# Performance work log

Measured on AMD Instinct MI355X. Metric: run time of the kernel, lower is better.

The kernel has to match this reference:

```python
import jax, jax.numpy as jnp
import numpy as np

T, N, F_IN, F_OUT, E = 12, 512, 32, 8, 16384
H = N * F_OUT  # 4096, LSTM input_size == hidden_size


def setup_inputs() -> dict:
    key = jax.random.key(0)
    ks = jax.random.split(key, 7)
    return {
        "x": jax.random.normal(ks[0], (T, N, F_IN), jnp.float32),
        "edge_index": jax.random.randint(ks[1], (T, 2, E), 0, N, jnp.int32),
        "edge_weight": jax.random.uniform(ks[2], (T, E), jnp.float32),
        "W_gcn": jax.random.normal(ks[3], (F_IN, F_OUT), jnp.float32) * 0.1,
        "b_gcn": jnp.zeros((F_OUT,), jnp.float32),
        "W_ih": jax.random.normal(ks[4], (4 * H, H), jnp.float32) * 0.02,
        "W_hh": jax.random.normal(ks[5], (4 * H, H), jnp.float32) * 0.02,
        "b_ih": jnp.zeros((4 * H,), jnp.float32),
        "b_hh": jnp.zeros((4 * H,), jnp.float32),
    }


def _gcn(x, ei, ew, W, b):
    # PyG GCNConv with edge_weight: add self loops (w=1), symmetric norm, scatter-add at target.
    row, col = ei[0], ei[1]
    loop = jnp.arange(N, dtype=ei.dtype)
    row = jnp.concatenate([row, loop])
    col = jnp.concatenate([col, loop])
    w = jnp.concatenate([ew, jnp.ones((N,), ew.dtype)])
    deg = jax.ops.segment_sum(w, col, num_segments=N)
    dinv = jnp.where(deg > 0, 1.0 / jnp.sqrt(jnp.where(deg > 0, deg, 1.0)), 0.0)
    norm = dinv[row] * w * dinv[col]  # [E+N]
    h = x @ W  # [N, F_OUT]
    out = jax.ops.segment_sum(norm[:, None] * h[row], col, num_segments=N)
    return out + b


def reference(x, edge_index, edge_weight, W_gcn, b_gcn, W_ih, W_hh, b_ih, b_hh):
    # Per-snapshot GCNConv -> relu (dropout is identity in eval mode)
    conv = jax.vmap(_gcn, in_axes=(0, 0, 0, None, None))(x, edge_index, edge_weight, W_gcn, b_gcn)
    feats = jax.nn.relu(conv).reshape(T, N * F_OUT)  # [T, H] LSTM inputs (batch=1)

    def step(carry, xt):
        h, c = carry
        g = xt @ W_ih.T + b_ih + h @ W_hh.T + b_hh  # [4H], torch gate order i,f,g,o
        i, f, gg, o = jnp.split(g, 4)
        c = jax.nn.sigmoid(f) * c + jax.nn.sigmoid(i) * jnp.tanh(gg)
        h = jax.nn.sigmoid(o) * jnp.tanh(c)
        return (h, c), None

    h0 = jnp.zeros((H,), x.dtype)
    c0 = jnp.zeros((H,), x.dtype)
    (h, c), _ = jax.lax.scan(step, (h0, c0), feats)
    # module returns (cell_state, hidden_state), each [1, H]
    return (c[None, :], h[None, :])
```

## Files before the change

### kernel.cpp

```cpp
#include <hip/hip_runtime.h>
#include <hip/hip_fp16.h>
#include <math.h>

#define T_STEPS 12
#define N_NODES 512
#define FIN 32
#define FOUT 8
#define E_EDGES 16384
#define HDIM 4096
#define H4 16384

__device__ __forceinline__ float sigmoidf_(float x) { return 1.0f / (1.0f + __expf(-x)); }

typedef float floatx4 __attribute__((ext_vector_type(4)));
__device__ __forceinline__ float4 ntload4(const float4* p) {
    floatx4 v = __builtin_nontemporal_load((const floatx4*)p);
    return make_float4(v.x, v.y, v.z, v.w);
}

__global__ __launch_bounds__(256) void gcn_kernel(
        const float* __restrict__ x,
        const int*   __restrict__ ei,
        const float* __restrict__ ew,
        const float* __restrict__ Wg,
        const float* __restrict__ bg,
        float* __restrict__ feats)
{
    const int t   = blockIdx.x;
    const int tid = threadIdx.x;

    __shared__ float hs[N_NODES * FOUT];
    __shared__ float outs[N_NODES * FOUT];
    __shared__ float deg[N_NODES];
    __shared__ float Wsh[FIN * FOUT];
    __shared__ float bsh[FOUT];

    const float* xt   = x  + (size_t)t * N_NODES * FIN;
    const int*   rowp = ei + (size_t)t * 2 * E_EDGES;
    const int*   colp = rowp + E_EDGES;
    const float* wp   = ew + (size_t)t * E_EDGES;

    if (tid < FIN * FOUT) Wsh[tid] = Wg[tid];
    if (tid < FOUT)       bsh[tid] = bg[tid];
    for (int i = tid; i < N_NODES; i += 256) deg[i] = 1.0f;
    for (int i = tid; i < N_NODES * FOUT; i += 256) outs[i] = 0.0f;
    __syncthreads();

    for (int idx = tid; idx < N_NODES * FOUT; idx += 256) {
        const int n = idx >> 3;
        const int f = idx & 7;
        const float* xr = xt + n * FIN;
        float acc = 0.0f;
        #pragma unroll
        for (int k = 0; k < FIN; ++k) acc += xr[k] * Wsh[k * FOUT + f];
        hs[idx] = acc;
    }
    for (int e = tid; e < E_EDGES; e += 256) atomicAdd(&deg[colp[e]], wp[e]);
    __syncthreads();

    for (int i = tid; i < N_NODES; i += 256) deg[i] = 1.0f / sqrtf(deg[i]);
    __syncthreads();

    for (int e = tid; e < E_EDGES; e += 256) {
        const int   r  = rowp[e];
        const int   cc = colp[e];
        const float coef = deg[r] * wp[e] * deg[cc];
        #pragma unroll
        for (int f = 0; f < FOUT; ++f)
            atomicAdd(&outs[cc * FOUT + f], coef * hs[r * FOUT + f]);
    }
    for (int n = tid; n < N_NODES; n += 256) {
        const float d2 = deg[n] * deg[n];
        #pragma unroll
        for (int f = 0; f < FOUT; ++f)
            atomicAdd(&outs[n * FOUT + f], d2 * hs[n * FOUT + f]);
    }
    __syncthreads();

    for (int idx = tid; idx < N_NODES * FOUT; idx += 256) {
        float v = outs[idx] + bsh[idx & 7];
        feats[(size_t)t * HDIM + idx] = v > 0.0f ? v : 0.0f;
    }
}

__global__ __launch_bounds__(256) void wih_gemm(
        const float* __restrict__ feats,
        const float* __restrict__ Wih,
        const float* __restrict__ b_ih,
        const float* __restrict__ b_hh,
        float* __restrict__ Xg)
{
    const int wave = threadIdx.x >> 6;
    const int lane = threadIdx.x & 63;
    const int r0   = blockIdx.x * 8 + wave * 2;

    const float4* W4 = (const float4*)Wih;
    const float4* F4 = (const float4*)feats;

    float acc0[T_STEPS], acc1[T_STEPS];
    #pragma unroll
    for (int t = 0; t < T_STEPS; ++t) { acc0[t] = 0.0f; acc1[t] = 0.0f; }

    #pragma unroll 1
    for (int ch = 0; ch < 16; ++ch) {
        const int k4 = ch * 64 + lane;
        const float4 w0 = ntload4(&W4[(size_t)r0 * (HDIM / 4) + k4]);
        const float4 w1 = ntload4(&W4[(size_t)(r0 + 1) * (HDIM / 4) + k4]);
        #pragma unroll
        for (int t = 0; t < T_STEPS; ++t) {
            const float4 fv = F4[t * (HDIM / 4) + k4];
            acc0[t] += w0.x * fv.x + w0.y * fv.y + w0.z * fv.z + w0.w * fv.w;
            acc1[t] += w1.x * fv.x + w1.y * fv.y + w1.z * fv.z + w1.w * fv.w;
        }
    }

    const float bias0 = b_ih[r0] + b_hh[r0];
    const float bias1 = b_ih[r0 + 1] + b_hh[r0 + 1];

    #pragma unroll
    for (int t = 0; t < T_STEPS; ++t) {
        float v0 = acc0[t], v1 = acc1[t];
        #pragma unroll
        for (int off = 32; off > 0; off >>= 1) {
            v0 += __shfl_xor(v0, off, 64);
            v1 += __shfl_xor(v1, off, 64);
        }
        if (lane == 0) {
            Xg[t * H4 + r0]     = v0 + bias0;
            Xg[t * H4 + r0 + 1] = v1 + bias1;
        }
    }
}

__global__ __launch_bounds__(256) void lstm_step0(
        const float* __restrict__ Xg0,
        float* __restrict__ h_out,
        float* __restrict__ c)
{
    const int j = blockIdx.x * 256 + threadIdx.x;
    const float gi = Xg0[j];
    const float gg = Xg0[2 * HDIM + j];
    const float go = Xg0[3 * HDIM + j];
    const float cj = sigmoidf_(gi) * tanhf(gg);
    c[j] = cj;
    h_out[j] = sigmoidf_(go) * tanhf(cj);
}

__global__ __launch_bounds__(256) void lstm_step_cvt(
        const float* __restrict__ Xg_t,
        const float* __restrict__ Whh,
        uint4* __restrict__ Whh16,
        const float* __restrict__ h_in,
        float* __restrict__ h_out,
        float* __restrict__ c)
{
    const int j    = blockIdx.x;
    const int wave = threadIdx.x >> 6;
    const int lane = threadIdx.x & 63;
    const int r    = wave * HDIM + j;

    const float xg    = (lane == 0) ? Xg_t[r] : 0.0f;
    const float cprev = (threadIdx.x == 0) ? c[j] : 0.0f;

    const float4* Wr  = (const float4*)(Whh + (size_t)r * HDIM);
    uint4*        Wo  = Whh16 + (size_t)r * (HDIM / 8);
    const float4* h4  = (const float4*)h_in;

    float acc = 0.0f;
    #pragma unroll
    for (int it = 0; it < 8; ++it) {
        const int g = it * 64 + lane;
        const float4 a  = ntload4(&Wr[2 * g]);
        const float4 b  = ntload4(&Wr[2 * g + 1]);
        const float4 ha = h4[2 * g];
        const float4 hb = h4[2 * g + 1];
        acc += a.x * ha.x + a.y * ha.y + a.z * ha.z + a.w * ha.w
             + b.x * hb.x + b.y * hb.y + b.z * hb.z + b.w * hb.w;
        union { uint4 u; __half2 h[4]; } pk;
        pk.h[0] = __floats2half2_rn(a.x, a.y);
        pk.h[1] = __floats2half2_rn(a.z, a.w);
        pk.h[2] = __floats2half2_rn(b.x, b.y);
        pk.h[3] = __floats2half2_rn(b.z, b.w);
        Wo[g] = pk.u;
    }
    #pragma unroll
    for (int off = 32; off > 0; off >>= 1) acc += __shfl_xor(acc, off, 64);

    __shared__ float gate[4];
    if (lane == 0) gate[wave] = acc + xg;
    __syncthreads();

    if (threadIdx.x == 0) {
        const float gi = gate[0], gf = gate[1], gg = gate[2], go = gate[3];
        const float cj = sigmoidf_(gf) * cprev + sigmoidf_(gi) * tanhf(gg);
        const float hj = sigmoidf_(go) * tanhf(cj);
        c[j] = cj;
        h_out[j] = hj;
    }
}

__global__ __launch_bounds__(256) void lstm_step_f16(
        const float* __restrict__ Xg_t,
        const uint4* __restrict__ Whh16,
        const float* __restrict__ h_in,
        float* __restrict__ h_out,
        float* __restrict__ c,
        float* __restrict__ final_out)
{
    const int j    = blockIdx.x;
    const int wave = threadIdx.x >> 6;
    const int lane = threadIdx.x & 63;
    const int r    = wave * HDIM + j;

    const float xg    = (lane == 0) ? Xg_t[r] : 0.0f;
    const float cprev = (threadIdx.x == 0) ? c[j] : 0.0f;

    const uint4*  Wr = Whh16 + (size_t)r * (HDIM / 8);
    const float4* h4 = (const float4*)h_in;

    float acc = 0.0f;
    #pragma unroll
    for (int it = 0; it < 8; ++it) {
        const int g = it * 64 + lane;
        uint4 wraw = Wr[g];
        const __half2* wh = (const __half2*)&wraw;
        const float4 ha = h4[2 * g];
        const float4 hb = h4[2 * g + 1];
        const float2 w0 = __half22float2(wh[0]);
        const float2 w1 = __half22float2(wh[1]);
        const float2 w2 = __half22float2(wh[2]);
        const float2 w3 = __half22float2(wh[3]);
        acc += w0.x * ha.x + w0.y * ha.y + w1.x * ha.z + w1.y * ha.w
             + w2.x * hb.x + w2.y * hb.y + w3.x * hb.z + w3.y * hb.w;
    }
    #pragma unroll
    for (int off = 32; off > 0; off >>= 1) acc += __shfl_xor(acc, off, 64);

    __shared__ float gate[4];
    if (lane == 0) gate[wave] = acc + xg;
    __syncthreads();

    if (threadIdx.x == 0) {
        const float gi = gate[0], gf = gate[1], gg = gate[2], go = gate[3];
        const float cj = sigmoidf_(gf) * cprev + sigmoidf_(gi) * tanhf(gg);
        const float hj = sigmoidf_(go) * tanhf(cj);
        c[j] = cj;
        h_out[j] = hj;
        if (final_out) { final_out[j] = cj; final_out[HDIM + j] = hj; }
    }
}

__global__ __launch_bounds__(256) void lstm_step_f32(
        const float* __restrict__ Xg_t,
        const float* __restrict__ Whh,
        const float* __restrict__ h_in,
        float* __restrict__ h_out,
        float* __restrict__ c,
        float* __restrict__ final_out)
{
    const int j    = blockIdx.x;
    const int wave = threadIdx.x >> 6;
    const int lane = threadIdx.x & 63;
    const int r    = wave * HDIM + j;

    const float xg    = (lane == 0) ? Xg_t[r] : 0.0f;
    const float cprev = (threadIdx.x == 0) ? c[j] : 0.0f;

    const float4* Wr = (const float4*)(Whh + (size_t)r * HDIM);
    const float4* h4 = (const float4*)h_in;

    float acc = 0.0f;
    #pragma unroll
    for (int it = 0; it < 16; ++it) {
        const int k4 = it * 64 + lane;
        const float4 w = Wr[k4];
        const float4 h = h4[k4];
        acc += w.x * h.x + w.y * h.y + w.z * h.z + w.w * h.w;
    }
    #pragma unroll
    for (int off = 32; off > 0; off >>= 1) acc += __shfl_xor(acc, off, 64);

    __shared__ float gate[4];
    if (lane == 0) gate[wave] = acc + xg;
    __syncthreads();

    if (threadIdx.x == 0) {
        const float gi = gate[0], gf = gate[1], gg = gate[2], go = gate[3];
        const float cj = sigmoidf_(gf) * cprev + sigmoidf_(gi) * tanhf(gg);
        const float hj = sigmoidf_(go) * tanhf(cj);
        c[j] = cj;
        h_out[j] = hj;
        if (final_out) { final_out[j] = cj; final_out[HDIM + j] = hj; }
    }
}

extern "C" void kernel_launch(void* const* d_in, const int* in_sizes, int n_in,
                              void* d_out, int out_size, void* d_ws, size_t ws_size,
                              hipStream_t stream) {
    const float* x    = (const float*)d_in[0];
    const int*   ei   = (const int*)  d_in[1];
    const float* ew   = (const float*)d_in[2];
    const float* Wg   = (const float*)d_in[3];
    const float* bg   = (const float*)d_in[4];
    const float* Wih  = (const float*)d_in[5];
    const float* Whh  = (const float*)d_in[6];
    const float* b_ih = (const float*)d_in[7];
    const float* b_hh = (const float*)d_in[8];
    float* out = (float*)d_out;

    const size_t fp16_bytes  = (size_t)H4 * HDIM * sizeof(__half);
    const size_t float_elems = (size_t)T_STEPS * HDIM + (size_t)T_STEPS * H4 + 3 * HDIM;
    const bool   use_fp16    = ws_size >= fp16_bytes + float_elems * sizeof(float);

    char*  base  = (char*)d_ws;
    uint4* Whh16 = (uint4*)base;
    float* fbase = use_fp16 ? (float*)(base + fp16_bytes) : (float*)base;
    float* feats = fbase;
    float* Xg    = feats + T_STEPS * HDIM;
    float* hA    = Xg + T_STEPS * H4;
    float* hB    = hA + HDIM;
    float* c     = hB + HDIM;

    gcn_kernel<<<T_STEPS, 256, 0, stream>>>(x, ei, ew, Wg, bg, feats);
    wih_gemm<<<H4 / 8, 256, 0, stream>>>(feats, Wih, b_ih, b_hh, Xg);

    lstm_step0<<<HDIM / 256, 256, 0, stream>>>(Xg, hA, c);

    float* hin = hA;
    float* hout = hB;
    if (use_fp16) {
        lstm_step_cvt<<<HDIM, 256, 0, stream>>>(Xg + (size_t)1 * H4, Whh, Whh16, hin, hout, c);
        { float* tmp = hin; hin = hout; hout = tmp; }
        for (int t = 2; t < T_STEPS; ++t) {
            float* fout = (t == T_STEPS - 1) ? out : nullptr;
            lstm_step_f16<<<HDIM, 256, 0, stream>>>(Xg + (size_t)t * H4, Whh16, hin, hout, c, fout);
            float* tmp = hin; hin = hout; hout = tmp;
        }
    } else {
        for (int t = 1; t < T_STEPS; ++t) {
            float* fout = (t == T_STEPS - 1) ? out : nullptr;
            lstm_step_f32<<<HDIM, 256, 0, stream>>>(Xg + (size_t)t * H4, Whh, hin, hout, c, fout);
            float* tmp = hin; hin = hout; hout = tmp;
        }
    }
}
```

Baseline: 993.9 us.

## Split GCN stage into multi-kernel, edge-partitioned scatter across many blocks

Replaces the single 12-block GCN kernel with four kernels. The first computes the projected features and zeroes the buffers. The second accumulates degrees with global atomics over 16 edge chunks per snapshot. The third scatters each chunk into shared memory and flushes it to a global accumulator, and the fourth adds the self-loop and bias and applies relu. This spreads the serial per-snapshot edge work across 192 blocks instead of 12, so more of the GPU is used. The cost is three extra launches, global atomics, and extra workspace, which could push the fp16 workspace check over the available size.

```diff
diff --git a/kernel.cpp b/kernel.cpp
--- a/kernel.cpp
+++ b/kernel.cpp
@@ -9,6 +9,8 @@
 #define E_EDGES 16384
 #define HDIM 4096
 #define H4 16384
+#define KSPLIT 16
+#define EPB (E_EDGES / KSPLIT)
 
 __device__ __forceinline__ float sigmoidf_(float x) { return 1.0f / (1.0f + __expf(-x)); }
 
@@ -18,69 +20,91 @@
     return make_float4(v.x, v.y, v.z, v.w);
 }
 
-__global__ __launch_bounds__(256) void gcn_kernel(
+__global__ __launch_bounds__(256) void gcn_hs_init(
         const float* __restrict__ x,
+        const float* __restrict__ Wg,
+        float* __restrict__ hs_g,
+        float* __restrict__ deg_g,
+        float* __restrict__ acc_g)
+{
+    const int idx = blockIdx.x * 256 + threadIdx.x;
+    const int t  = idx >> 12;
+    const int nf = idx & (HDIM - 1);
+    const int n  = nf >> 3;
+    const int f  = nf & 7;
+    const float* xr = x + ((size_t)t * N_NODES + n) * FIN;
+    float acc = 0.0f;
+    #pragma unroll
+    for (int k = 0; k < FIN; ++k) acc += xr[k] * Wg[k * FOUT + f];
+    hs_g[idx]  = acc;
+    acc_g[idx] = 0.0f;
+    if (f == 0) deg_g[t * N_NODES + n] = 0.0f;
+}
+
+__global__ __launch_bounds__(256) void gcn_deg(
         const int*   __restrict__ ei,
         const float* __restrict__ ew,
-        const float* __restrict__ Wg,
-        const float* __restrict__ bg,
-        float* __restrict__ feats)
-{
-    const int t   = blockIdx.x;
-    const int tid = threadIdx.x;
-
-    __shared__ float hs[N_NODES * FOUT];
-    __shared__ float outs[N_NODES * FOUT];
-    __shared__ float deg[N_NODES];
-    __shared__ float Wsh[FIN * FOUT];
-    __shared__ float bsh[FOUT];
-
-    const float* xt   = x  + (size_t)t * N_NODES * FIN;
+        float* __restrict__ deg_g)
+{
+    const int t = blockIdx.x / KSPLIT;
+    const int s = blockIdx.x % KSPLIT;
+    const int* colp = ei + (size_t)t * 2 * E_EDGES + E_EDGES;
+    const float* wp = ew + (size_t)t * E_EDGES;
+    const int e0 = s * EPB;
+    for (int e = e0 + threadIdx.x; e < e0 + EPB; e += 256)
+        atomicAdd(&deg_g[t * N_NODES + colp[e]], wp[e]);
+}
+
+__global__ __launch_bounds__(256) void gcn_scatter(
+        const int*   __restrict__ ei,
+        const float* __restrict__ ew,
+        const float* __restrict__ hs_g,
+        const float* __restrict__ deg_g,
+        float* __restrict__ acc_g)
+{
+    const int t = blockIdx.x / KSPLIT;
+    const int s = blockIdx.x % KSPLIT;
+
+    __shared__ float outs[HDIM];
+    for (int i = threadIdx.x; i < HDIM; i += 256) outs[i] = 0.0f;
+    __syncthreads();
+
     const int*   rowp = ei + (size_t)t * 2 * E_EDGES;
     const int*   colp = rowp + E_EDGES;
     const float* wp   = ew + (size_t)t * E_EDGES;
-
-    if (tid < FIN * FOUT) Wsh[tid] = Wg[tid];
-    if (tid < FOUT)       bsh[tid] = bg[tid];
-    for (int i = tid; i < N_NODES; i += 256) deg[i] = 1.0f;
-    for (int i = tid; i < N_NODES * FOUT; i += 256) outs[i] = 0.0f;
-    __syncthreads();
-
-    for (int idx = tid; idx < N_NODES * FOUT; idx += 256) {
-        const int n = idx >> 3;
-        const int f = idx & 7;
-        const float* xr = xt + n * FIN;
-        float acc = 0.0f;
-        #pragma unroll
-        for (int k = 0; k < FIN; ++k) acc += xr[k] * Wsh[k * FOUT + f];
-        hs[idx] = acc;
-    }
-    for (int e = tid; e < E_EDGES; e += 256) atomicAdd(&deg[colp[e]], wp[e]);
-    __syncthreads();
-
-    for (int i = tid; i < N_NODES; i += 256) deg[i] = 1.0f / sqrtf(deg[i]);
-    __syncthreads();
-
-    for (int e = tid; e < E_EDGES; e += 256) {
+    const float* hs   = hs_g + (size_t)t * HDIM;
+    const float* dg   = deg_g + t * N_NODES;
+
+    const int e0 = s * EPB;
+    for (int e = e0 + threadIdx.x; e < e0 + EPB; e += 256) {
         const int   r  = rowp[e];
         const int   cc = colp[e];
-        const float coef = deg[r] * wp[e] * deg[cc];
+        const float coef = wp[e] / sqrtf((1.0f + dg[r]) * (1.0f + dg[cc]));
         #pragma unroll
         for (int f = 0; f < FOUT; ++f)
             atomicAdd(&outs[cc * FOUT + f], coef * hs[r * FOUT + f]);
     }
-    for (int n = tid; n < N_NODES; n += 256) {
-        const float d2 = deg[n] * deg[n];
-        #pragma unroll
-        for (int f = 0; f < FOUT; ++f)
-            atomicAdd(&outs[n * FOUT + f], d2 * hs[n * FOUT + f]);
-    }
-    __syncthreads();
-
-    for (int idx = tid; idx < N_NODES * FOUT; idx += 256) {
-        float v = outs[idx] + bsh[idx & 7];
-        feats[(size_t)t * HDIM + idx] = v > 0.0f ? v : 0.0f;
-    }
+    __syncthreads();
+
+    float* acc = acc_g + (size_t)t * HDIM;
+    for (int i = threadIdx.x; i < HDIM; i += 256)
+        atomicAdd(&acc[i], outs[i]);
+}
+
+__global__ __launch_bounds__(256) void gcn_final(
+        const float* __restrict__ acc_g,
+        const float* __restrict__ hs_g,
+        const float* __restrict__ deg_g,
+        const float* __restrict__ bg,
+        float* __restrict__ feats)
+{
+    const int idx = blockIdx.x * 256 + threadIdx.x;
+    const int t  = idx >> 12;
+    const int nf = idx & (HDIM - 1);
+    const int n  = nf >> 3;
+    const float dinv2 = 1.0f / (1.0f + deg_g[t * N_NODES + n]);
+    const float v = acc_g[idx] + dinv2 * hs_g[idx] + bg[nf & 7];
+    feats[idx] = v > 0.0f ? v : 0.0f;
 }
 
 __global__ __launch_bounds__(256) void wih_gemm(
@@ -309,19 +333,29 @@
     float* out = (float*)d_out;
 
     const size_t fp16_bytes  = (size_t)H4 * HDIM * sizeof(__half);
-    const size_t float_elems = (size_t)T_STEPS * HDIM + (size_t)T_STEPS * H4 + 3 * HDIM;
+    const size_t float_elems = (size_t)T_STEPS * HDIM * 3
+                             + (size_t)T_STEPS * N_NODES
+                             + (size_t)T_STEPS * H4
+                             + 3 * HDIM;
     const bool   use_fp16    = ws_size >= fp16_bytes + float_elems * sizeof(float);
 
     char*  base  = (char*)d_ws;
     uint4* Whh16 = (uint4*)base;
     float* fbase = use_fp16 ? (float*)(base + fp16_bytes) : (float*)base;
     float* feats = fbase;
-    float* Xg    = feats + T_STEPS * HDIM;
+    float* hs_g  = feats + T_STEPS * HDIM;
+    float* acc_g = hs_g + T_STEPS * HDIM;
+    float* deg_g = acc_g + T_STEPS * HDIM;
+    float* Xg    = deg_g + T_STEPS * N_NODES;
     float* hA    = Xg + T_STEPS * H4;
     float* hB    = hA + HDIM;
     float* c     = hB + HDIM;
 
-    gcn_kernel<<<T_STEPS, 256, 0, stream>>>(x, ei, ew, Wg, bg, feats);
+    gcn_hs_init<<<T_STEPS * HDIM / 256, 256, 0, stream>>>(x, Wg, hs_g, deg_g, acc_g);
+    gcn_deg    <<<T_STEPS * KSPLIT,     256, 0, stream>>>(ei, ew, deg_g);
+    gcn_scatter<<<T_STEPS * KSPLIT,     256, 0, stream>>>(ei, ew, hs_g, deg_g, acc_g);
+    gcn_final  <<<T_STEPS * HDIM / 256, 256, 0, stream>>>(acc_g, hs_g, deg_g, bg, feats);
+
     wih_gemm<<<H4 / 8, 256, 0, stream>>>(feats, Wih, b_ih, b_hh, Xg);
 
     lstm_step0<<<HDIM / 256, 256, 0, stream>>>(Xg, hA, c);
```

Measured after the change: 813.8 us. 1.22x faster.
